# Kernel optimization log

Hardware: AMD Instinct MI355X
Metric: run time of the kernel (lower is better)

The kernel has to match this reference:

```python
import jax, jax.numpy as jnp
import numpy as np

C = 256
NUM_HEADS = 4


def setup_inputs() -> dict:
    key = jax.random.key(0)
    ks = jax.random.split(key, 7)
    B, H, W = 4, 64, 64
    s = 1.0 / np.sqrt(C)
    return {
        "x": jax.random.normal(ks[0], (B, C, H, W), dtype=jnp.float32),
        "ln_gamma": jnp.ones((C,), jnp.float32),
        "ln_beta": jnp.zeros((C,), jnp.float32),
        "w_qkv": jax.random.normal(ks[1], (C, 3 * C), dtype=jnp.float32) * s,
        "b_qkv": jnp.zeros((3 * C,), jnp.float32),
        "w_proj": jax.random.normal(ks[2], (C, C), dtype=jnp.float32) * s,
        "b_proj": jnp.zeros((C,), jnp.float32),
    }


def reference(x, ln_gamma, ln_beta, w_qkv, b_qkv, w_proj, b_proj):
    B, Cc, H, W = x.shape
    N = H * W
    hd = Cc // NUM_HEADS
    # [B, N, C] token layout
    x_ = jnp.transpose(x, (0, 2, 3, 1)).reshape(B, N, Cc)
    # LayerNorm over channel dim
    mu = jnp.mean(x_, axis=-1, keepdims=True)
    var = jnp.mean(jnp.square(x_ - mu), axis=-1, keepdims=True)
    xn = (x_ - mu) * jax.lax.rsqrt(var + 1e-5) * ln_gamma + ln_beta
    qkv = xn @ w_qkv + b_qkv  # [B, N, 3C]
    q, k, v = jnp.split(qkv, 3, axis=-1)
    # [B, heads, N, hd]
    q = q.reshape(B, N, NUM_HEADS, hd).transpose(0, 2, 1, 3)
    k = k.reshape(B, N, NUM_HEADS, hd).transpose(0, 2, 1, 3)
    v = v.reshape(B, N, NUM_HEADS, hd).transpose(0, 2, 1, 3)
    # NOTE: source scales by 1/sqrt(C), not 1/sqrt(head_dim)
    scores = jnp.einsum("bhnd,bhmd->bhnm", q, k) / jnp.sqrt(jnp.float32(Cc))
    attn = jax.nn.softmax(scores, axis=-1)
    out = jnp.einsum("bhnm,bhmd->bhnd", attn, v)
    out = out.transpose(0, 2, 1, 3).reshape(B, N, Cc)
    out = out @ w_proj + b_proj
    out = out.reshape(B, H, W, Cc).transpose(0, 3, 1, 2)
    return x + out
```

## Files before the change

### kernel.cpp

```cpp
#include <hip/hip_runtime.h>
#include <hip/hip_bf16.h>

typedef __bf16 bf16_t;
typedef bf16_t bf16x8 __attribute__((ext_vector_type(8)));
typedef bf16_t bf16x4v __attribute__((ext_vector_type(4)));
typedef float f32x4 __attribute__((ext_vector_type(4)));
typedef float f32x16 __attribute__((ext_vector_type(16)));
typedef int i32x4 __attribute__((ext_vector_type(4)));

constexpr int C = 256;
constexpr int Bb = 4;
constexpr int N = 4096;
constexpr int NH = 4;
constexpr int HD = 64;
constexpr float SM_SCALE_LOG2E = 0.0625f * 1.44269504088896340736f;

__device__ __forceinline__ int swz_chunk(int row, int chunk) {
  return row * 128 + ((chunk ^ (row & 7)) << 4);
}

__device__ __forceinline__ f32x4 mfma16(bf16x8 a, bf16x8 b, f32x4 c) {
  return __builtin_amdgcn_mfma_f32_16x16x32_bf16(a, b, c, 0, 0, 0);
}
__device__ __forceinline__ f32x16 mfma32(bf16x8 a, bf16x8 b, f32x16 c) {
  return __builtin_amdgcn_mfma_f32_32x32x16_bf16(a, b, c, 0, 0, 0);
}

__global__ __launch_bounds__(256, 2) void ln_kernel(
    const float* __restrict__ x, const float* __restrict__ gamma,
    const float* __restrict__ beta, bf16_t* __restrict__ xn) {
  __shared__ float tile[256][65];
  __shared__ float red[2][4][64];
  __shared__ float mu_s[64], rs_s[64];
  int tid = threadIdx.x, lane = tid & 63, wv = tid >> 6;
  int b = blockIdx.x >> 6;
  int n0 = (blockIdx.x & 63) << 6;
  const float* xb = x + ((size_t)b * C) * N + n0;
  #pragma unroll 4
  for (int i = 0; i < 64; ++i) {
    int c = wv * 64 + i;
    tile[c][lane] = xb[(size_t)c * N + lane];
  }
  __syncthreads();
  float s = 0.f, s2 = 0.f;
  #pragma unroll 8
  for (int i = 0; i < 64; ++i) {
    float v = tile[wv * 64 + i][lane];
    s += v; s2 += v * v;
  }
  red[0][wv][lane] = s; red[1][wv][lane] = s2;
  __syncthreads();
  if (tid < 64) {
    float ts  = red[0][0][tid] + red[0][1][tid] + red[0][2][tid] + red[0][3][tid];
    float ts2 = red[1][0][tid] + red[1][1][tid] + red[1][2][tid] + red[1][3][tid];
    float mu  = ts * (1.f / 256.f);
    float var = fmaxf(ts2 * (1.f / 256.f) - mu * mu, 0.f);
    mu_s[tid] = mu;
    rs_s[tid] = rsqrtf(var + 1e-5f);
  }
  __syncthreads();
  float g = gamma[tid], be = beta[tid];
  bf16_t* xo = xn + ((size_t)(b * N + n0)) * C + tid;
  #pragma unroll 4
  for (int i = 0; i < 64; ++i) {
    float v = (tile[tid][i] - mu_s[i]) * rs_s[i] * g + be;
    xo[(size_t)i * C] = (bf16_t)v;
  }
}

__global__ void conv_w(const float* __restrict__ wqkv, const float* __restrict__ wproj,
                       bf16_t* __restrict__ wqkvT, bf16_t* __restrict__ wprojT) {
  int id = blockIdx.x * 256 + threadIdx.x;
  if (id < 768 * 256) {
    int nn = id >> 8, kk = id & 255;
    wqkvT[id] = (bf16_t)wqkv[(size_t)kk * 768 + nn];
  }
  if (id < 256 * 256) {
    int nn = id >> 8, kk = id & 255;
    wprojT[id] = (bf16_t)wproj[(size_t)kk * 256 + nn];
  }
}

__global__ __launch_bounds__(256, 4) void gemm_qkv(
    const bf16_t* __restrict__ xn, const bf16_t* __restrict__ wT,
    const float* __restrict__ bias,
    bf16_t* __restrict__ Q, bf16_t* __restrict__ K, bf16_t* __restrict__ Vt) {
  __shared__ char smem[2 * 8192];
  char* As = smem;
  char* Bs = smem + 8192;
  int tid = threadIdx.x, lane = tid & 63, wv = tid >> 6;
  int mt = blockIdx.x & 255, nt = blockIdx.x >> 8;
  int m0 = mt * 64, ncol0 = nt * 64;
  f32x4 acc[4];
  #pragma unroll
  for (int i = 0; i < 4; ++i) acc[i] = (f32x4){0.f, 0.f, 0.f, 0.f};
  for (int kt = 0; kt < 4; ++kt) {
    int k0 = kt * 64;
    __syncthreads();
    #pragma unroll
    for (int it = 0; it < 2; ++it) {
      int idx = it * 256 + tid, row = idx >> 3, cb = idx & 7;
      *(i32x4*)(As + swz_chunk(row, cb)) =
          *(const i32x4*)(xn + (size_t)(m0 + row) * C + k0 + cb * 8);
      *(i32x4*)(Bs + swz_chunk(row, cb)) =
          *(const i32x4*)(wT + (size_t)(ncol0 + row) * C + k0 + cb * 8);
    }
    __syncthreads();
    int r = wv * 16 + (lane & 15), q = lane >> 4;
    bf16x8 a0 = *(const bf16x8*)(As + swz_chunk(r, q));
    bf16x8 a1 = *(const bf16x8*)(As + swz_chunk(r, 4 + q));
    #pragma unroll
    for (int ct = 0; ct < 4; ++ct) {
      int br = ct * 16 + (lane & 15);
      bf16x8 b0 = *(const bf16x8*)(Bs + swz_chunk(br, q));
      bf16x8 b1 = *(const bf16x8*)(Bs + swz_chunk(br, 4 + q));
      acc[ct] = mfma16(a0, b0, acc[ct]);
      acc[ct] = mfma16(a1, b1, acc[ct]);
    }
  }
  #pragma unroll
  for (int ct = 0; ct < 4; ++ct) {
    int cg = ncol0 + ct * 16 + (lane & 15);
    float bv = bias[cg];
    int sect = cg >> 8;
    int cc = cg & 255;
    int h = cc >> 6, d = cc & 63;
    #pragma unroll
    for (int j = 0; j < 4; ++j) {
      int m = m0 + wv * 16 + (lane >> 4) * 4 + j;
      int b_ = m >> 12, n = m & 4095;
      float v = acc[ct][j] + bv;
      if (sect == 0) {
        Q[((size_t)((b_ * NH + h) * N + n)) * HD + d] = (bf16_t)(v * SM_SCALE_LOG2E);
      } else if (sect == 1) {
        K[((size_t)((b_ * NH + h) * N + n)) * HD + d] = (bf16_t)v;
      } else {
        Vt[((size_t)((b_ * NH + h) * HD + d)) * N + n] = (bf16_t)v;
      }
    }
  }
}

__global__ __launch_bounds__(512, 4) void attn_kernel(
    const bf16_t* __restrict__ Q, const bf16_t* __restrict__ K,
    const bf16_t* __restrict__ Vt, bf16_t* __restrict__ aout) {
  __shared__ char smem[65536];
  char* tiles = smem;
  char* QP = smem + 32768;
  int tid = threadIdx.x, lane = tid & 63, wv = tid >> 6;
  int hi = lane >> 5, qL = lane & 31;
  int wq = wv >> 1, par = wv & 1;
  int bh = blockIdx.x >> 5, qt = blockIdx.x & 31;
  int q0 = qt * 128;

  const bf16_t* Qbase = Q + ((size_t)bh * N + q0) * HD;
  #pragma unroll
  for (int it = 0; it < 2; ++it) {
    int idx = it * 512 + tid;
    int row = idx >> 3, cb = idx & 7;
    *(i32x4*)(QP + swz_chunk(row, cb)) =
        *(const i32x4*)(Qbase + (size_t)row * HD + cb * 8);
  }
  __syncthreads();
  bf16x8 qb[4];
  #pragma unroll
  for (int hs = 0; hs < 4; ++hs)
    qb[hs] = *(const bf16x8*)(QP + swz_chunk(wq * 32 + qL, hs * 2 + hi));

  char* kbase = tiles + par * 16384;
  char* vbase = kbase + 8192;
  char* pstrip = QP + wv * 4096;
  const bf16_t* Kbh = K + (size_t)bh * N * HD;
  const bf16_t* Vbh = Vt + (size_t)bh * HD * N;

  float m_r = -3.0e38f, l_r = 0.f;
  f32x16 o0, o1;
  #pragma unroll
  for (int i = 0; i < 16; ++i) { o0[i] = 0.f; o1[i] = 0.f; }

  int srow = tid >> 3, scb = tid & 7;
  for (int adv = 0; adv < 32; ++adv) {
    int n0 = adv * 128;
    {
      const bf16_t* s0p = Kbh + (size_t)(n0 + srow) * HD + scb * 8;
      const bf16_t* s1p = Vbh + (size_t)srow * N + n0 + scb * 8;
      const bf16_t* s2p = Kbh + (size_t)(n0 + 64 + srow) * HD + scb * 8;
      const bf16_t* s3p = Vbh + (size_t)srow * N + n0 + 64 + scb * 8;
      int d = swz_chunk(srow, scb);
      *(i32x4*)(tiles + d)         = *(const i32x4*)s0p;
      *(i32x4*)(tiles + 8192 + d)  = *(const i32x4*)s1p;
      *(i32x4*)(tiles + 16384 + d) = *(const i32x4*)s2p;
      *(i32x4*)(tiles + 24576 + d) = *(const i32x4*)s3p;
    }
    __syncthreads();
    f32x16 s0, s1;
    #pragma unroll
    for (int i = 0; i < 16; ++i) { s0[i] = 0.f; s1[i] = 0.f; }
    #pragma unroll
    for (int hs = 0; hs < 4; ++hs) {
      bf16x8 ka0 = *(const bf16x8*)(kbase + swz_chunk(qL, hs * 2 + hi));
      bf16x8 ka1 = *(const bf16x8*)(kbase + swz_chunk(32 + qL, hs * 2 + hi));
      s0 = mfma32(ka0, qb[hs], s0);
      s1 = mfma32(ka1, qb[hs], s1);
    }
    float tm = s0[0];
    #pragma unroll
    for (int i = 1; i < 16; ++i) tm = fmaxf(tm, s0[i]);
    #pragma unroll
    for (int i = 0; i < 16; ++i) tm = fmaxf(tm, s1[i]);
    tm = fmaxf(tm, __shfl_xor(tm, 32));
    float nm = fmaxf(m_r, tm);
    if (!__all(nm == m_r)) {
      float f = __builtin_amdgcn_exp2f(m_r - nm);
      l_r *= f;
      o0 *= f; o1 *= f;
      m_r = nm;
    }
    float rs = 0.f;
    #pragma unroll
    for (int i = 0; i < 16; ++i) {
      float p = __builtin_amdgcn_exp2f(s0[i] - m_r); s0[i] = p; rs += p;
    }
    #pragma unroll
    for (int i = 0; i < 16; ++i) {
      float p = __builtin_amdgcn_exp2f(s1[i] - m_r); s1[i] = p; rs += p;
    }
    rs += __shfl_xor(rs, 32);
    l_r += rs;
    #pragma unroll
    for (int g = 0; g < 4; ++g) {
      bf16x4v p0, p1;
      #pragma unroll
      for (int j = 0; j < 4; ++j) {
        p0[j] = (bf16_t)s0[g * 4 + j];
        p1[j] = (bf16_t)s1[g * 4 + j];
      }
      *(bf16x4v*)(pstrip + swz_chunk(qL, g) + hi * 8) = p0;
      *(bf16x4v*)(pstrip + swz_chunk(qL, 4 + g) + hi * 8) = p1;
    }
    #pragma unroll
    for (int t16 = 0; t16 < 4; ++t16) {
      bf16x8 pb  = *(const bf16x8*)(pstrip + swz_chunk(qL, t16 * 2 + hi));
      bf16x8 va0 = *(const bf16x8*)(vbase + swz_chunk(qL, t16 * 2 + hi));
      bf16x8 va1 = *(const bf16x8*)(vbase + swz_chunk(32 + qL, t16 * 2 + hi));
      o0 = mfma32(va0, pb, o0);
      o1 = mfma32(va1, pb, o1);
    }
    __syncthreads();
  }

  float* mlb = (float*)smem;
  if (hi == 0) {
    mlb[(wv * 32 + qL) * 2]     = m_r;
    mlb[(wv * 32 + qL) * 2 + 1] = l_r;
  }
  __syncthreads();
  float m_p = mlb[((wv ^ 1) * 32 + qL) * 2];
  float l_p = mlb[((wv ^ 1) * 32 + qL) * 2 + 1];
  float M = fmaxf(m_r, m_p);
  float w_s = __builtin_amdgcn_exp2f(m_r - M);
  float l_tot = l_r * w_s + l_p * __builtin_amdgcn_exp2f(m_p - M);
  char* obuf = smem + 2048 + wq * 8192;
  if (par == 0) {
    #pragma unroll
    for (int g = 0; g < 8; ++g) {
      f32x4 t;
      #pragma unroll
      for (int j = 0; j < 4; ++j)
        t[j] = (g < 4 ? o0[g * 4 + j] : o1[(g - 4) * 4 + j]) * w_s;
      *(f32x4*)(obuf + swz_chunk(lane, g)) = t;
    }
  }
  __syncthreads();
  if (par == 1) {
    float inv = 1.f / l_tot;
    int qglob = q0 + wq * 32 + qL;
    int b_ = bh >> 2, h = bh & 3;
    bf16_t* ab = aout + ((size_t)b_ * N + qglob) * C + h * HD;
    #pragma unroll
    for (int g = 0; g < 8; ++g) {
      f32x4 part = *(const f32x4*)(obuf + swz_chunk(lane, g));
      int hdb = g >> 2, gg = g & 3;
      bf16x4v ov;
      #pragma unroll
      for (int j = 0; j < 4; ++j) {
        float own = hdb ? o1[gg * 4 + j] : o0[gg * 4 + j];
        ov[j] = (bf16_t)((part[j] + own * w_s) * inv);
      }
      *(bf16x4v*)(ab + hdb * 32 + gg * 8 + hi * 4) = ov;
    }
  }
}

__global__ __launch_bounds__(256, 4) void gemm_proj(
    const bf16_t* __restrict__ aout, const bf16_t* __restrict__ wT,
    const float* __restrict__ bias, const float* __restrict__ x,
    float* __restrict__ out) {
  __shared__ char smem[2 * 8192];
  char* As = smem;
  char* Bs = smem + 8192;
  int tid = threadIdx.x, lane = tid & 63, wv = tid >> 6;
  int mt = blockIdx.x & 255, nt = blockIdx.x >> 8;
  int m0 = mt * 64, c0 = nt * 64;
  f32x4 acc[4];
  #pragma unroll
  for (int i = 0; i < 4; ++i) acc[i] = (f32x4){0.f, 0.f, 0.f, 0.f};
  for (int kt = 0; kt < 4; ++kt) {
    int k0 = kt * 64;
    __syncthreads();
    #pragma unroll
    for (int it = 0; it < 2; ++it) {
      int idx = it * 256 + tid, row = idx >> 3, cb = idx & 7;
      *(i32x4*)(As + swz_chunk(row, cb)) =
          *(const i32x4*)(aout + (size_t)(m0 + row) * C + k0 + cb * 8);
      *(i32x4*)(Bs + swz_chunk(row, cb)) =
          *(const i32x4*)(wT + (size_t)(c0 + row) * C + k0 + cb * 8);
    }
    __syncthreads();
    int r = wv * 16 + (lane & 15), q = lane >> 4;
    bf16x8 a0 = *(const bf16x8*)(As + swz_chunk(r, q));
    bf16x8 a1 = *(const bf16x8*)(As + swz_chunk(r, 4 + q));
    #pragma unroll
    for (int ct = 0; ct < 4; ++ct) {
      int br = ct * 16 + (lane & 15);
      bf16x8 b0 = *(const bf16x8*)(Bs + swz_chunk(br, q));
      bf16x8 b1 = *(const bf16x8*)(Bs + swz_chunk(br, 4 + q));
      acc[ct] = mfma16(a0, b0, acc[ct]);
      acc[ct] = mfma16(a1, b1, acc[ct]);
    }
  }
  #pragma unroll
  for (int ct = 0; ct < 4; ++ct) {
    int c = c0 + ct * 16 + (lane & 15);
    float bv = bias[c];
    int m = m0 + wv * 16 + (lane >> 4) * 4;
    int b_ = m >> 12, n = m & 4095;
    size_t off = ((size_t)(b_ * C + c)) * N + n;
    f32x4 xin = *(const f32x4*)(x + off);
    f32x4 res;
    #pragma unroll
    for (int j = 0; j < 4; ++j) res[j] = xin[j] + acc[ct][j] + bv;
    *(f32x4*)(out + off) = res;
  }
}

extern "C" void kernel_launch(void* const* d_in, const int* in_sizes, int n_in,
                              void* d_out, int out_size, void* d_ws, size_t ws_size,
                              hipStream_t stream) {
  const float* x     = (const float*)d_in[0];
  const float* gam   = (const float*)d_in[1];
  const float* bet   = (const float*)d_in[2];
  const float* wqkv  = (const float*)d_in[3];
  const float* bqkv  = (const float*)d_in[4];
  const float* wproj = (const float*)d_in[5];
  const float* bproj = (const float*)d_in[6];
  float* out = (float*)d_out;

  char* ws = (char*)d_ws;
  size_t off = 0;
  auto alloc = [&](size_t bytes) {
    void* p = ws + off;
    off += (bytes + 255) & ~(size_t)255;
    return p;
  };
  bf16_t* xn     = (bf16_t*)alloc((size_t)Bb * N * C * 2);
  bf16_t* wqkvT  = (bf16_t*)alloc((size_t)768 * 256 * 2);
  bf16_t* wprojT = (bf16_t*)alloc((size_t)256 * 256 * 2);
  bf16_t* Qb     = (bf16_t*)alloc((size_t)Bb * NH * N * HD * 2);
  bf16_t* Kb     = (bf16_t*)alloc((size_t)Bb * NH * N * HD * 2);
  bf16_t* Vtb    = (bf16_t*)alloc((size_t)Bb * NH * HD * N * 2);
  bf16_t* aout   = (bf16_t*)alloc((size_t)Bb * N * C * 2);
  if (ws_size < off) return;

  hipLaunchKernelGGL(ln_kernel, dim3(Bb * 64), dim3(256), 0, stream, x, gam, bet, xn);
  hipLaunchKernelGGL(conv_w, dim3(768), dim3(256), 0, stream, wqkv, wproj, wqkvT, wprojT);
  hipLaunchKernelGGL(gemm_qkv, dim3(256 * 12), dim3(256), 0, stream, xn, wqkvT, bqkv,
                     Qb, Kb, Vtb);
  hipLaunchKernelGGL(attn_kernel, dim3(16 * 32), dim3(512), 0, stream,
                     Qb, Kb, Vtb, aout);
  hipLaunchKernelGGL(gemm_proj, dim3(256 * 4), dim3(256), 0, stream, aout, wprojT,
                     bproj, x, out);
}
```

Before: 214.8 us.

## Register-prefetch K/V tiles and pass P via permlane swap instead of LDS

The attention loop now prefetches the next K/V tile into registers while the current one is computed, so global load latency overlaps the MFMA work. The P matrix is repacked in registers with v_cvt_pk_bf16 and permlane32_swap instead of going through an LDS strip, and the cross-half max and sum reductions also use permlane swaps. Dropping the LDS strip cuts shared memory from 64 KB to about 34 KB, which could allow more blocks per CU. In exchange the kernel holds more live registers, the output buffer is reused after the loop, and correctness depends on the permlane lane mapping matching the MFMA B-operand layout.

```diff
diff --git a/kernel.cpp b/kernel.cpp
--- a/kernel.cpp
+++ b/kernel.cpp
@@ -7,6 +7,7 @@
 typedef float f32x4 __attribute__((ext_vector_type(4)));
 typedef float f32x16 __attribute__((ext_vector_type(16)));
 typedef int i32x4 __attribute__((ext_vector_type(4)));
+typedef int i32x2 __attribute__((ext_vector_type(2)));
 
 constexpr int C = 256;
 constexpr int Bb = 4;
@@ -24,6 +25,23 @@
 }
 __device__ __forceinline__ f32x16 mfma32(bf16x8 a, bf16x8 b, f32x16 c) {
   return __builtin_amdgcn_mfma_f32_32x32x16_bf16(a, b, c, 0, 0, 0);
+}
+
+__device__ __forceinline__ int cvt_pk_bf16(float lo, float hi) {
+  int d;
+  asm("v_cvt_pk_bf16_f32 %0, %1, %2" : "=v"(d) : "v"(lo), "v"(hi));
+  return d;
+}
+__device__ __forceinline__ i32x2 plswap(int a, int b) {
+  return __builtin_amdgcn_permlane32_swap(a, b, false, false);
+}
+__device__ __forceinline__ float xhalf_max(float v) {
+  i32x2 r = plswap(__float_as_int(v), __float_as_int(v));
+  return fmaxf(__int_as_float(r[0]), __int_as_float(r[1]));
+}
+__device__ __forceinline__ float xhalf_sum(float v) {
+  i32x2 r = plswap(__float_as_int(v), __float_as_int(v));
+  return __int_as_float(r[0]) + __int_as_float(r[1]);
 }
 
 __global__ __launch_bounds__(256, 2) void ln_kernel(
@@ -144,55 +162,60 @@
 __global__ __launch_bounds__(512, 4) void attn_kernel(
     const bf16_t* __restrict__ Q, const bf16_t* __restrict__ K,
     const bf16_t* __restrict__ Vt, bf16_t* __restrict__ aout) {
-  __shared__ char smem[65536];
+  __shared__ char smem[34816];
   char* tiles = smem;
-  char* QP = smem + 32768;
   int tid = threadIdx.x, lane = tid & 63, wv = tid >> 6;
   int hi = lane >> 5, qL = lane & 31;
   int wq = wv >> 1, par = wv & 1;
   int bh = blockIdx.x >> 5, qt = blockIdx.x & 31;
   int q0 = qt * 128;
 
+  const bf16_t* Kbh = K + (size_t)bh * N * HD;
+  const bf16_t* Vbh = Vt + (size_t)bh * HD * N;
+  int srow = tid >> 3, scb = tid & 7;
+  int sd = swz_chunk(srow, scb);
+
+  i32x4 st0 = *(const i32x4*)(Kbh + (size_t)srow * HD + scb * 8);
+  i32x4 st1 = *(const i32x4*)(Vbh + (size_t)srow * N + scb * 8);
+  i32x4 st2 = *(const i32x4*)(Kbh + (size_t)(64 + srow) * HD + scb * 8);
+  i32x4 st3 = *(const i32x4*)(Vbh + (size_t)srow * N + 64 + scb * 8);
+
   const bf16_t* Qbase = Q + ((size_t)bh * N + q0) * HD;
   #pragma unroll
   for (int it = 0; it < 2; ++it) {
     int idx = it * 512 + tid;
     int row = idx >> 3, cb = idx & 7;
-    *(i32x4*)(QP + swz_chunk(row, cb)) =
+    *(i32x4*)(tiles + swz_chunk(row, cb)) =
         *(const i32x4*)(Qbase + (size_t)row * HD + cb * 8);
   }
   __syncthreads();
   bf16x8 qb[4];
   #pragma unroll
   for (int hs = 0; hs < 4; ++hs)
-    qb[hs] = *(const bf16x8*)(QP + swz_chunk(wq * 32 + qL, hs * 2 + hi));
+    qb[hs] = *(const bf16x8*)(tiles + swz_chunk(wq * 32 + qL, hs * 2 + hi));
+  __syncthreads();
 
   char* kbase = tiles + par * 16384;
   char* vbase = kbase + 8192;
-  char* pstrip = QP + wv * 4096;
-  const bf16_t* Kbh = K + (size_t)bh * N * HD;
-  const bf16_t* Vbh = Vt + (size_t)bh * HD * N;
 
   float m_r = -3.0e38f, l_r = 0.f;
   f32x16 o0, o1;
   #pragma unroll
   for (int i = 0; i < 16; ++i) { o0[i] = 0.f; o1[i] = 0.f; }
 
-  int srow = tid >> 3, scb = tid & 7;
   for (int adv = 0; adv < 32; ++adv) {
-    int n0 = adv * 128;
-    {
-      const bf16_t* s0p = Kbh + (size_t)(n0 + srow) * HD + scb * 8;
-      const bf16_t* s1p = Vbh + (size_t)srow * N + n0 + scb * 8;
-      const bf16_t* s2p = Kbh + (size_t)(n0 + 64 + srow) * HD + scb * 8;
-      const bf16_t* s3p = Vbh + (size_t)srow * N + n0 + 64 + scb * 8;
-      int d = swz_chunk(srow, scb);
-      *(i32x4*)(tiles + d)         = *(const i32x4*)s0p;
-      *(i32x4*)(tiles + 8192 + d)  = *(const i32x4*)s1p;
-      *(i32x4*)(tiles + 16384 + d) = *(const i32x4*)s2p;
-      *(i32x4*)(tiles + 24576 + d) = *(const i32x4*)s3p;
-    }
-    __syncthreads();
+    *(i32x4*)(tiles + sd)         = st0;
+    *(i32x4*)(tiles + 8192 + sd)  = st1;
+    *(i32x4*)(tiles + 16384 + sd) = st2;
+    *(i32x4*)(tiles + 24576 + sd) = st3;
+    __syncthreads();
+    if (adv < 31) {
+      int n1 = (adv + 1) * 128;
+      st0 = *(const i32x4*)(Kbh + (size_t)(n1 + srow) * HD + scb * 8);
+      st1 = *(const i32x4*)(Vbh + (size_t)srow * N + n1 + scb * 8);
+      st2 = *(const i32x4*)(Kbh + (size_t)(n1 + 64 + srow) * HD + scb * 8);
+      st3 = *(const i32x4*)(Vbh + (size_t)srow * N + n1 + 64 + scb * 8);
+    }
     f32x16 s0, s1;
     #pragma unroll
     for (int i = 0; i < 16; ++i) { s0[i] = 0.f; s1[i] = 0.f; }
@@ -208,7 +231,7 @@
     for (int i = 1; i < 16; ++i) tm = fmaxf(tm, s0[i]);
     #pragma unroll
     for (int i = 0; i < 16; ++i) tm = fmaxf(tm, s1[i]);
-    tm = fmaxf(tm, __shfl_xor(tm, 32));
+    tm = xhalf_max(tm);
     float nm = fmaxf(m_r, tm);
     if (!__all(nm == m_r)) {
       float f = __builtin_amdgcn_exp2f(m_r - nm);
@@ -225,31 +248,34 @@
     for (int i = 0; i < 16; ++i) {
       float p = __builtin_amdgcn_exp2f(s1[i] - m_r); s1[i] = p; rs += p;
     }
-    rs += __shfl_xor(rs, 32);
-    l_r += rs;
-    #pragma unroll
-    for (int g = 0; g < 4; ++g) {
-      bf16x4v p0, p1;
-      #pragma unroll
-      for (int j = 0; j < 4; ++j) {
-        p0[j] = (bf16_t)s0[g * 4 + j];
-        p1[j] = (bf16_t)s1[g * 4 + j];
+    l_r += xhalf_sum(rs);
+    #pragma unroll
+    for (int t16 = 0; t16 < 4; ++t16) {
+      int dE0, dE1, dO0, dO1;
+      if (t16 < 2) {
+        dE0 = cvt_pk_bf16(s0[t16 * 8 + 0], s0[t16 * 8 + 1]);
+        dE1 = cvt_pk_bf16(s0[t16 * 8 + 2], s0[t16 * 8 + 3]);
+        dO0 = cvt_pk_bf16(s0[t16 * 8 + 4], s0[t16 * 8 + 5]);
+        dO1 = cvt_pk_bf16(s0[t16 * 8 + 6], s0[t16 * 8 + 7]);
+      } else {
+        dE0 = cvt_pk_bf16(s1[(t16 - 2) * 8 + 0], s1[(t16 - 2) * 8 + 1]);
+        dE1 = cvt_pk_bf16(s1[(t16 - 2) * 8 + 2], s1[(t16 - 2) * 8 + 3]);
+        dO0 = cvt_pk_bf16(s1[(t16 - 2) * 8 + 4], s1[(t16 - 2) * 8 + 5]);
+        dO1 = cvt_pk_bf16(s1[(t16 - 2) * 8 + 6], s1[(t16 - 2) * 8 + 7]);
       }
-      *(bf16x4v*)(pstrip + swz_chunk(qL, g) + hi * 8) = p0;
-      *(bf16x4v*)(pstrip + swz_chunk(qL, 4 + g) + hi * 8) = p1;
-    }
-    #pragma unroll
-    for (int t16 = 0; t16 < 4; ++t16) {
-      bf16x8 pb  = *(const bf16x8*)(pstrip + swz_chunk(qL, t16 * 2 + hi));
+      i32x2 rA = plswap(dE0, dO0);
+      i32x2 rB = plswap(dE1, dO1);
+      union { i32x4 i; bf16x8 h; } u;
+      u.i = (i32x4){rA[0], rB[0], rA[1], rB[1]};
       bf16x8 va0 = *(const bf16x8*)(vbase + swz_chunk(qL, t16 * 2 + hi));
       bf16x8 va1 = *(const bf16x8*)(vbase + swz_chunk(32 + qL, t16 * 2 + hi));
-      o0 = mfma32(va0, pb, o0);
-      o1 = mfma32(va1, pb, o1);
-    }
-    __syncthreads();
-  }
-
-  float* mlb = (float*)smem;
+      o0 = mfma32(va0, u.h, o0);
+      o1 = mfma32(va1, u.h, o1);
+    }
+    __syncthreads();
+  }
+
+  float* mlb = (float*)(smem + 32768);
   if (hi == 0) {
     mlb[(wv * 32 + qL) * 2]     = m_r;
     mlb[(wv * 32 + qL) * 2 + 1] = l_r;
@@ -260,7 +286,7 @@
   float M = fmaxf(m_r, m_p);
   float w_s = __builtin_amdgcn_exp2f(m_r - M);
   float l_tot = l_r * w_s + l_p * __builtin_amdgcn_exp2f(m_p - M);
-  char* obuf = smem + 2048 + wq * 8192;
+  char* obuf = smem + wq * 8192;
   if (par == 0) {
     #pragma unroll
     for (int g = 0; g < 8; ++g) {
```

After: 208.6 us. 1.03x faster.
